# Kernel optimization log

Measured on AMD Instinct MI355X. Metric: run time of the kernel, lower is better.

## Reference

```python
import jax, jax.numpy as jnp
import numpy as np

N, E, D, H, L = 40000, 640000, 128, 4, 2
C = D // H  # head dim
NEG_SLOPE = 0.2


def setup_inputs() -> dict:
    key = jax.random.key(0)
    ks = jax.random.split(key, 9)
    s = 1.0 / np.sqrt(D)
    x = jax.random.normal(ks[0], (N, D), dtype=jnp.float32)
    edge_index = jax.random.randint(ks[1], (2, E), 0, N, dtype=jnp.int64)
    # Per-layer stacked GATv2Conv parameters (PyG parameterization):
    Wl = jax.random.normal(ks[2], (L, D, D), dtype=jnp.float32) * s   # lin_l weight
    bl = jnp.zeros((L, D), dtype=jnp.float32)                          # lin_l bias
    Wr = jax.random.normal(ks[3], (L, D, D), dtype=jnp.float32) * s   # lin_r weight
    br = jnp.zeros((L, D), dtype=jnp.float32)                          # lin_r bias
    att = jax.random.normal(ks[4], (L, H, C), dtype=jnp.float32) * (1.0 / np.sqrt(C))
    Wres = jax.random.normal(ks[5], (L, D, D), dtype=jnp.float32) * s  # residual proj
    bias = jnp.zeros((L, D), dtype=jnp.float32)                        # final bias
    return {"x": x, "edge_index": edge_index, "Wl": Wl, "bl": bl,
            "Wr": Wr, "br": br, "att": att, "Wres": Wres, "bias": bias}


def _gatv2_layer(x, src, dst, Wl, bl, Wr, br, att, Wres, b):
    # x: [N, D]; src/dst: [E] (edge j -> i, dst is aggregation target)
    xl = (x @ Wl + bl).reshape(N, H, C)
    xr = (x @ Wr + br).reshape(N, H, C)
    # per-edge GATv2 score: a^T LeakyReLU(xl_j + xr_i)
    e = jax.nn.leaky_relu(xl[src] + xr[dst], NEG_SLOPE)        # [E, H, C]
    alpha = jnp.einsum('ehc,hc->eh', e, att)                    # [E, H]
    # segment softmax over edges grouped by target node
    amax = jax.ops.segment_max(alpha, dst, num_segments=N)      # [N, H]
    amax = jnp.where(jnp.isfinite(amax), amax, 0.0)
    ex = jnp.exp(alpha - amax[dst])
    denom = jax.ops.segment_sum(ex, dst, num_segments=N) + 1e-16
    a = ex / denom[dst]                                         # [E, H]
    # scatter-add weighted source messages
    out = jax.ops.segment_sum(xl[src] * a[:, :, None], dst, num_segments=N)
    out = out.reshape(N, H * C) + x @ Wres + b                  # concat heads + residual + bias
    return jax.nn.elu(out)


def reference(x, edge_index, Wl, bl, Wr, br, att, Wres, bias):
    src, dst = edge_index[0], edge_index[1]
    for l in range(L):
        x = _gatv2_layer(x, src, dst, Wl[l], bl[l], Wr[l], br[l], att[l], Wres[l], bias[l])
    return x
```

## Files before the change

### kernel.cpp

```cpp
#include <hip/hip_runtime.h>
#include <cstdint>

#define NN 40000
#define EE 640000
#define DD 128
#define HH 4
#define CC 32
#define LL 2
#define NEG_SLOPE 0.2f
#define NBLK 157

typedef __attribute__((ext_vector_type(8))) short bf16x8;
typedef __attribute__((ext_vector_type(4))) float f32x4;
typedef __attribute__((ext_vector_type(2))) float f32x2;

__device__ __forceinline__ unsigned short f2bf(float f) {
    unsigned u = __float_as_uint(f);
    unsigned r = (u + 0x7FFFu + ((u >> 16) & 1)) >> 16;
    return (unsigned short)r;
}
__device__ __forceinline__ float bf2f(unsigned short u) {
    return __uint_as_float(((unsigned)u) << 16);
}

__device__ __forceinline__ void gload16(const void* g, void* l) {
    __builtin_amdgcn_global_load_lds(
        (const __attribute__((address_space(1))) unsigned*)g,
        (__attribute__((address_space(3))) unsigned*)l, 16, 0, 0);
}

template<int CTRL>
__device__ __forceinline__ float dpp_badd(float v) {
    const int j = __builtin_amdgcn_mov_dpp(__float_as_int(v), CTRL, 0xF, 0xF, true);
    return v + __int_as_float(j);
}

__global__ __launch_bounds__(256) void prep_kernel(
    const float* __restrict__ x,
    const float* __restrict__ Wl, const float* __restrict__ Wr,
    const float* __restrict__ Wres,
    unsigned short* __restrict__ xb, unsigned short* __restrict__ Wb,
    int* __restrict__ deg)
{
    const int i = blockIdx.x * 256 + threadIdx.x;
    if (i < NN * DD / 4) {
        const float4 v = ((const float4*)x)[i];
        ushort4 o;
        o.x = f2bf(v.x); o.y = f2bf(v.y); o.z = f2bf(v.z); o.w = f2bf(v.w);
        ((ushort4*)xb)[i] = o;
    }
    if (i < LL * 6 * 8192) {
        const int l = i / 49152;
        const int rem0 = i - l * 49152;
        const int nb = rem0 >> 13;
        const int rem = rem0 & 8191;
        const int q = rem >> 9;
        const int n = (rem >> 3) & 63;
        const int j = rem & 7;
        const int k = q * 8 + j;
        const int colg = (nb & 1) * 64 + n;
        const float* W = (nb < 2) ? Wl : (nb < 4) ? Wr : Wres;
        Wb[i] = f2bf(W[(size_t)l * DD * DD + k * DD + colg]);
    }
    if (i < NN) deg[i] = 0;
}

__global__ __launch_bounds__(256) void gemm_mfma_kernel(
    const unsigned short* __restrict__ xb, const unsigned short* __restrict__ Wb,
    const float* __restrict__ bl, const float* __restrict__ br,
    const float* __restrict__ bias,
    unsigned short* __restrict__ xlb, unsigned short* __restrict__ xrb,
    unsigned short* __restrict__ resb)
{
    __shared__ __align__(16) unsigned short lds[16384];
    const int lane = threadIdx.x & 63;
    const int wv = threadIdx.x >> 6;
    const int row0 = blockIdx.x << 6;

#pragma unroll
    for (int j = 0; j < 4; ++j) {
        const int q = j * 4 + wv;
        gload16(xb + (size_t)(row0 + lane) * DD + q * 8, &lds[q * 512]);
    }

    const int wm = wv >> 1, wn = wv & 1;
    const int h = lane >> 4, r = lane & 15;

    for (int t = 0; t < 6; ++t) {
        __syncthreads();
#pragma unroll
        for (int j = 0; j < 4; ++j) {
            const int q = j * 4 + wv;
            gload16(Wb + (size_t)t * 8192 + q * 512 + lane * 8, &lds[8192 + q * 512]);
        }
        __syncthreads();

        f32x4 acc[2][2] = {{{0.f,0.f,0.f,0.f},{0.f,0.f,0.f,0.f}},
                           {{0.f,0.f,0.f,0.f},{0.f,0.f,0.f,0.f}}};
#pragma unroll
        for (int s = 0; s < 4; ++s) {
            const int base = (s * 4 + h) * 64;
            const bf16x8 a0 = *(const bf16x8*)&lds[(base + wm * 32 + r) * 8];
            const bf16x8 a1 = *(const bf16x8*)&lds[(base + wm * 32 + 16 + r) * 8];
            const bf16x8 b0 = *(const bf16x8*)&lds[8192 + (base + wn * 32 + r) * 8];
            const bf16x8 b1 = *(const bf16x8*)&lds[8192 + (base + wn * 32 + 16 + r) * 8];
            acc[0][0] = __builtin_amdgcn_mfma_f32_16x16x32_bf16(a0, b0, acc[0][0], 0, 0, 0);
            acc[0][1] = __builtin_amdgcn_mfma_f32_16x16x32_bf16(a0, b1, acc[0][1], 0, 0, 0);
            acc[1][0] = __builtin_amdgcn_mfma_f32_16x16x32_bf16(a1, b0, acc[1][0], 0, 0, 0);
            acc[1][1] = __builtin_amdgcn_mfma_f32_16x16x32_bf16(a1, b1, acc[1][1], 0, 0, 0);
        }

        unsigned short* const outp = (t < 2) ? xlb : (t < 4) ? xrb : resb;
        const float* const bp = (t < 2) ? bl : (t < 4) ? br : bias;
        const int c0 = (t & 1) * 64 + wn * 32;
#pragma unroll
        for (int ni = 0; ni < 2; ++ni) {
            const int col = c0 + ni * 16 + r;
            const float bv = bp[col];
#pragma unroll
            for (int mi = 0; mi < 2; ++mi) {
                const int rw = row0 + wm * 32 + mi * 16 + h * 4;
#pragma unroll
                for (int v = 0; v < 4; ++v)
                    outp[(size_t)(rw + v) * DD + col] = f2bf(acc[mi][ni][v] + bv);
            }
        }
    }
}


__global__ __launch_bounds__(256) void hist_kernel(
    const int* __restrict__ dst, int* __restrict__ deg)
{
    const int e = blockIdx.x * 256 + threadIdx.x;
    if (e < EE) atomicAdd(&deg[dst[e]], 1);
}

__global__ __launch_bounds__(256) void scan1_kernel(
    const int* __restrict__ deg, int* __restrict__ rowptr, int* __restrict__ blksum)
{
    __shared__ int s[256];
    const int i = blockIdx.x * 256 + threadIdx.x;
    const int v = (i < NN) ? deg[i] : 0;
    s[threadIdx.x] = v;
    __syncthreads();
    for (int off = 1; off < 256; off <<= 1) {
        const int t = (threadIdx.x >= off) ? s[threadIdx.x - off] : 0;
        __syncthreads();
        s[threadIdx.x] += t;
        __syncthreads();
    }
    if (i < NN) rowptr[i] = s[threadIdx.x] - v;
    if (threadIdx.x == 255) blksum[blockIdx.x] = s[255];
}

__global__ __launch_bounds__(256) void scan23_kernel(
    int* __restrict__ rowptr, const int* __restrict__ blksum, int* __restrict__ cursor)
{
    __shared__ int s[256];
    const int v = (threadIdx.x < NBLK) ? blksum[threadIdx.x] : 0;
    s[threadIdx.x] = v;
    __syncthreads();
    for (int off = 1; off < 256; off <<= 1) {
        const int t = (threadIdx.x >= off) ? s[threadIdx.x - off] : 0;
        __syncthreads();
        s[threadIdx.x] += t;
        __syncthreads();
    }
    const int boff = s[blockIdx.x] - blksum[blockIdx.x];
    const int i = blockIdx.x * 256 + threadIdx.x;
    if (i < NN) {
        const int val = rowptr[i] + boff;
        rowptr[i] = val;
        cursor[i] = val;
    }
    if (i == 0) rowptr[NN] = EE;
}

__global__ __launch_bounds__(256) void fill_kernel(
    const int* __restrict__ src, const int* __restrict__ dst,
    int* __restrict__ cursor, int* __restrict__ colb)
{
    const int e = blockIdx.x * 256 + threadIdx.x;
    if (e < EE) {
        const int p = atomicAdd(&cursor[dst[e]], 1);
        colb[p] = src[e] << 8;
    }
}

__global__ __launch_bounds__(64) void gather_kernel(
    const unsigned short* __restrict__ xlb, const unsigned short* __restrict__ xrb,
    const unsigned short* __restrict__ resb,
    const int* __restrict__ rowptr, const int* __restrict__ colb,
    const float* __restrict__ att,
    float* __restrict__ outf, unsigned short* __restrict__ outb)
{
    const int node = blockIdx.x;
    const int lane = threadIdx.x;
    const int halfid = lane >> 5;
    const int hl = lane & 31;

    const uint2 xu = *(const uint2*)(xrb + (size_t)node * DD + hl * 4);
    const f32x2 xr01 = {__uint_as_float(xu.x << 16), __uint_as_float(xu.x & 0xFFFF0000u)};
    const f32x2 xr23 = {__uint_as_float(xu.y << 16), __uint_as_float(xu.y & 0xFFFF0000u)};
    const float4 attv = ((const float4*)att)[hl];
    const f32x2 at6_01 = {0.6f * attv.x, 0.6f * attv.y};
    const f32x2 at6_23 = {0.6f * attv.z, 0.6f * attv.w};
    const f32x2 at4_01 = {0.4f * attv.x, 0.4f * attv.y};
    const f32x2 at4_23 = {0.4f * attv.z, 0.4f * attv.w};
    const char* const xbase = (const char*)xlb;

    float d = 0.f;
    f32x2 acc01 = {0.f, 0.f}, acc23 = {0.f, 0.f};
    const int beg = rowptr[node], end = rowptr[node + 1];

    int p = beg;

#define CHUNK_BODY(GUARDED)                                                    \
    {                                                                          \
        f32x2 xv01[4], xv23[4]; float al[4]; int vl[4];                        \
        _Pragma("unroll")                                                      \
        for (int i = 0; i < 4; ++i) {                                          \
            const int q = p + 2 * i + halfid;                                  \
            vl[i] = GUARDED ? (q < end) : 1;                                   \
            const int off = colb[vl[i] ? q : beg];                             \
            const uint2 u = *(const uint2*)(xbase + off + hl * 8);             \
            xv01[i] = (f32x2){__uint_as_float(u.x << 16),                      \
                              __uint_as_float(u.x & 0xFFFF0000u)};             \
            xv23[i] = (f32x2){__uint_as_float(u.y << 16),                      \
                              __uint_as_float(u.y & 0xFFFF0000u)};             \
        }                                                                      \
        _Pragma("unroll")                                                      \
        for (int i = 0; i < 4; ++i) {                                          \
            const f32x2 z01 = xv01[i] + xr01;                                  \
            const f32x2 z23 = xv23[i] + xr23;                                  \
            const f32x2 za01 = __builtin_elementwise_abs(z01);                 \
            const f32x2 za23 = __builtin_elementwise_abs(z23);                 \
            f32x2 s2 = z01 * at6_01;                                           \
            s2 += za01 * at4_01;                                               \
            s2 += z23 * at6_23;                                                \
            s2 += za23 * at4_23;                                               \
            al[i] = s2.x + s2.y;                                               \
        }                                                                      \
        _Pragma("unroll")                                                      \
        for (int i = 0; i < 4; ++i) {                                          \
            al[i] = dpp_badd<0xB1>(al[i]);      \
            al[i] = dpp_badd<0x4E>(al[i]);      \
            al[i] = dpp_badd<0x141>(al[i]);     \
        }                                                                      \
        _Pragma("unroll")                                                      \
        for (int i = 0; i < 4; ++i) {                                          \
            float w = __expf(al[i]);                                           \
            if (GUARDED) w = vl[i] ? w : 0.f;                                  \
            const f32x2 w2 = {w, w};                                           \
            d += w;                                                            \
            acc01 += w2 * xv01[i];                                             \
            acc23 += w2 * xv23[i];                                             \
        }                                                                      \
    }

    for (; p + 8 <= end; p += 8) CHUNK_BODY(0)
    if (p < end) CHUNK_BODY(1)
#undef CHUNK_BODY

    d += __shfl_xor(d, 32);
    acc01.x += __shfl_xor(acc01.x, 32); acc01.y += __shfl_xor(acc01.y, 32);
    acc23.x += __shfl_xor(acc23.x, 32); acc23.y += __shfl_xor(acc23.y, 32);

    if (halfid == 0) {
        const float inv = 1.f / (d + 1e-16f);
        const ushort4 ru = ((const ushort4*)(resb + (size_t)node * DD))[hl];
        float o0 = acc01.x * inv + bf2f(ru.x);
        float o1 = acc01.y * inv + bf2f(ru.y);
        float o2 = acc23.x * inv + bf2f(ru.z);
        float o3 = acc23.y * inv + bf2f(ru.w);
        o0 = (o0 > 0.f) ? o0 : expm1f(o0);
        o1 = (o1 > 0.f) ? o1 : expm1f(o1);
        o2 = (o2 > 0.f) ? o2 : expm1f(o2);
        o3 = (o3 > 0.f) ? o3 : expm1f(o3);
        if (outf) {
            float4 ov; ov.x = o0; ov.y = o1; ov.z = o2; ov.w = o3;
            ((float4*)(outf + (size_t)node * DD))[hl] = ov;
        }
        if (outb) {
            ushort4 ob;
            ob.x = f2bf(o0); ob.y = f2bf(o1); ob.z = f2bf(o2); ob.w = f2bf(o3);
            ((ushort4*)(outb + (size_t)node * DD))[hl] = ob;
        }
    }
}

extern "C" void kernel_launch(void* const* d_in, const int* in_sizes, int n_in,
                              void* d_out, int out_size, void* d_ws, size_t ws_size,
                              hipStream_t stream)
{
    const float* x0   = (const float*)d_in[0];
    const int*   ei   = (const int*)  d_in[1];
    const float* Wl   = (const float*)d_in[2];
    const float* bl   = (const float*)d_in[3];
    const float* Wr   = (const float*)d_in[4];
    const float* br   = (const float*)d_in[5];
    const float* att  = (const float*)d_in[6];
    const float* Wres = (const float*)d_in[7];
    const float* bias = (const float*)d_in[8];
    const int* src = ei;
    const int* dst = ei + EE;

    float* p = (float*)d_ws;
    unsigned short* xlb  = (unsigned short*)p; p += (size_t)NN * DD / 2;
    unsigned short* xrb  = (unsigned short*)p; p += (size_t)NN * DD / 2;
    unsigned short* resb = (unsigned short*)p; p += (size_t)NN * DD / 2;
    unsigned short* xb0  = (unsigned short*)p; p += (size_t)NN * DD / 2;
    unsigned short* xb1  = (unsigned short*)p; p += (size_t)NN * DD / 2;
    unsigned short* Wb   = (unsigned short*)p; p += LL * 6 * 8192 / 2;
    int* rowptr = (int*)p; p += NN + 1;
    int* deg    = (int*)p; p += NN;
    int* cursor = (int*)p; p += NN;
    int* blksum = (int*)p; p += NBLK;
    int* colb   = (int*)p; p += EE;

    prep_kernel<<<(NN * DD / 4 + 255) / 256, 256, 0, stream>>>(
        x0, Wl, Wr, Wres, xb0, Wb, deg);
    hist_kernel<<<(EE + 255) / 256, 256, 0, stream>>>(dst, deg);
    scan1_kernel<<<NBLK, 256, 0, stream>>>(deg, rowptr, blksum);
    scan23_kernel<<<NBLK, 256, 0, stream>>>(rowptr, blksum, cursor);
    fill_kernel<<<(EE + 255) / 256, 256, 0, stream>>>(src, dst, cursor, colb);

    for (int l = 0; l < LL; ++l) {
        const unsigned short* xin = (l == 0) ? xb0 : xb1;
        gemm_mfma_kernel<<<625, 256, 0, stream>>>(
            xin, Wb + (size_t)l * 6 * 8192, bl + l * DD, br + l * DD, bias + l * DD,
            xlb, xrb, resb);
        gather_kernel<<<NN, 64, 0, stream>>>(
            xlb, xrb, resb, rowptr, colb, att + (size_t)l * HH * CC,
            (l == LL - 1) ? (float*)d_out : nullptr,
            (l == 0) ? xb1 : nullptr);
    }
}
```

Measured before the change: 167.3 us.

## Record per-edge atomic rank in histogram and fuse CSR fill into first GEMM

The histogram kernel now stores each edge's atomic return value as its rank within its destination bucket. The CSR fill then needs no second atomic pass: it writes colb[rowptr[dst]+rank] directly. That fill runs as extra blocks appended to the layer-0 GEMM launch, which removes one kernel launch and lets the fill overlap with the MFMA work. In exchange the change adds a 2.5MB rank buffer that must be written and then read back. The neighbor order inside each bucket still depends on atomic ordering, as before.

```diff
diff --git a/kernel.cpp b/kernel.cpp
--- a/kernel.cpp
+++ b/kernel.cpp
@@ -65,14 +65,67 @@
     if (i < NN) deg[i] = 0;
 }
 
+__global__ __launch_bounds__(256) void rank_kernel(
+    const int* __restrict__ dst, int* __restrict__ deg, int* __restrict__ rank)
+{
+    const int e = blockIdx.x * 256 + threadIdx.x;
+    if (e < EE) rank[e] = atomicAdd(&deg[dst[e]], 1);
+}
+
+__global__ __launch_bounds__(256) void scan1_kernel(
+    const int* __restrict__ deg, int* __restrict__ rowptr, int* __restrict__ blksum)
+{
+    __shared__ int s[256];
+    const int i = blockIdx.x * 256 + threadIdx.x;
+    const int v = (i < NN) ? deg[i] : 0;
+    s[threadIdx.x] = v;
+    __syncthreads();
+    for (int off = 1; off < 256; off <<= 1) {
+        const int t = (threadIdx.x >= off) ? s[threadIdx.x - off] : 0;
+        __syncthreads();
+        s[threadIdx.x] += t;
+        __syncthreads();
+    }
+    if (i < NN) rowptr[i] = s[threadIdx.x] - v;
+    if (threadIdx.x == 255) blksum[blockIdx.x] = s[255];
+}
+
+__global__ __launch_bounds__(256) void scan23_kernel(
+    int* __restrict__ rowptr, const int* __restrict__ blksum)
+{
+    __shared__ int s[256];
+    const int v = (threadIdx.x < NBLK) ? blksum[threadIdx.x] : 0;
+    s[threadIdx.x] = v;
+    __syncthreads();
+    for (int off = 1; off < 256; off <<= 1) {
+        const int t = (threadIdx.x >= off) ? s[threadIdx.x - off] : 0;
+        __syncthreads();
+        s[threadIdx.x] += t;
+        __syncthreads();
+    }
+    const int boff = s[blockIdx.x] - blksum[blockIdx.x];
+    const int i = blockIdx.x * 256 + threadIdx.x;
+    if (i < NN) rowptr[i] = rowptr[i] + boff;
+    if (i == 0) rowptr[NN] = EE;
+}
+
 __global__ __launch_bounds__(256) void gemm_mfma_kernel(
     const unsigned short* __restrict__ xb, const unsigned short* __restrict__ Wb,
     const float* __restrict__ bl, const float* __restrict__ br,
     const float* __restrict__ bias,
     unsigned short* __restrict__ xlb, unsigned short* __restrict__ xrb,
-    unsigned short* __restrict__ resb)
+    unsigned short* __restrict__ resb,
+    const int* __restrict__ src, const int* __restrict__ dst,
+    const int* __restrict__ rank, const int* __restrict__ rowptr,
+    int* __restrict__ colb)
 {
     __shared__ __align__(16) unsigned short lds[16384];
+    const int fb = (int)blockIdx.x - 625;
+    if (fb >= 0) {
+        const int e = fb * 256 + threadIdx.x;
+        if (e < EE) colb[rowptr[dst[e]] + rank[e]] = src[e] << 8;
+        return;
+    }
     const int lane = threadIdx.x & 63;
     const int wv = threadIdx.x >> 6;
     const int row0 = blockIdx.x << 6;
@@ -125,66 +178,6 @@
                     outp[(size_t)(rw + v) * DD + col] = f2bf(acc[mi][ni][v] + bv);
             }
         }
-    }
-}
-
-
-__global__ __launch_bounds__(256) void hist_kernel(
-    const int* __restrict__ dst, int* __restrict__ deg)
-{
-    const int e = blockIdx.x * 256 + threadIdx.x;
-    if (e < EE) atomicAdd(&deg[dst[e]], 1);
-}
-
-__global__ __launch_bounds__(256) void scan1_kernel(
-    const int* __restrict__ deg, int* __restrict__ rowptr, int* __restrict__ blksum)
-{
-    __shared__ int s[256];
-    const int i = blockIdx.x * 256 + threadIdx.x;
-    const int v = (i < NN) ? deg[i] : 0;
-    s[threadIdx.x] = v;
-    __syncthreads();
-    for (int off = 1; off < 256; off <<= 1) {
-        const int t = (threadIdx.x >= off) ? s[threadIdx.x - off] : 0;
-        __syncthreads();
-        s[threadIdx.x] += t;
-        __syncthreads();
-    }
-    if (i < NN) rowptr[i] = s[threadIdx.x] - v;
-    if (threadIdx.x == 255) blksum[blockIdx.x] = s[255];
-}
-
-__global__ __launch_bounds__(256) void scan23_kernel(
-    int* __restrict__ rowptr, const int* __restrict__ blksum, int* __restrict__ cursor)
-{
-    __shared__ int s[256];
-    const int v = (threadIdx.x < NBLK) ? blksum[threadIdx.x] : 0;
-    s[threadIdx.x] = v;
-    __syncthreads();
-    for (int off = 1; off < 256; off <<= 1) {
-        const int t = (threadIdx.x >= off) ? s[threadIdx.x - off] : 0;
-        __syncthreads();
-        s[threadIdx.x] += t;
-        __syncthreads();
-    }
-    const int boff = s[blockIdx.x] - blksum[blockIdx.x];
-    const int i = blockIdx.x * 256 + threadIdx.x;
-    if (i < NN) {
-        const int val = rowptr[i] + boff;
-        rowptr[i] = val;
-        cursor[i] = val;
-    }
-    if (i == 0) rowptr[NN] = EE;
-}
-
-__global__ __launch_bounds__(256) void fill_kernel(
-    const int* __restrict__ src, const int* __restrict__ dst,
-    int* __restrict__ cursor, int* __restrict__ colb)
-{
-    const int e = blockIdx.x * 256 + threadIdx.x;
-    if (e < EE) {
-        const int p = atomicAdd(&cursor[dst[e]], 1);
-        colb[p] = src[e] << 8;
     }
 }
 
@@ -315,22 +308,22 @@
     unsigned short* Wb   = (unsigned short*)p; p += LL * 6 * 8192 / 2;
     int* rowptr = (int*)p; p += NN + 1;
     int* deg    = (int*)p; p += NN;
-    int* cursor = (int*)p; p += NN;
+    int* rank   = (int*)p; p += EE;
     int* blksum = (int*)p; p += NBLK;
     int* colb   = (int*)p; p += EE;
 
     prep_kernel<<<(NN * DD / 4 + 255) / 256, 256, 0, stream>>>(
         x0, Wl, Wr, Wres, xb0, Wb, deg);
-    hist_kernel<<<(EE + 255) / 256, 256, 0, stream>>>(dst, deg);
+    rank_kernel<<<(EE + 255) / 256, 256, 0, stream>>>(dst, deg, rank);
     scan1_kernel<<<NBLK, 256, 0, stream>>>(deg, rowptr, blksum);
-    scan23_kernel<<<NBLK, 256, 0, stream>>>(rowptr, blksum, cursor);
-    fill_kernel<<<(EE + 255) / 256, 256, 0, stream>>>(src, dst, cursor, colb);
+    scan23_kernel<<<NBLK, 256, 0, stream>>>(rowptr, blksum);
 
     for (int l = 0; l < LL; ++l) {
         const unsigned short* xin = (l == 0) ? xb0 : xb1;
-        gemm_mfma_kernel<<<625, 256, 0, stream>>>(
+        const int fillBlocks = (l == 0) ? (EE + 255) / 256 : 0;
+        gemm_mfma_kernel<<<625 + fillBlocks, 256, 0, stream>>>(
             xin, Wb + (size_t)l * 6 * 8192, bl + l * DD, br + l * DD, bias + l * DD,
-            xlb, xrb, resb);
+            xlb, xrb, resb, src, dst, rank, rowptr, colb);
         gather_kernel<<<NN, 64, 0, stream>>>(
             xlb, xrb, resb, rowptr, colb, att + (size_t)l * HH * CC,
             (l == LL - 1) ? (float*)d_out : nullptr,
```

After: 140.8 us. -15.8%, faster.
